# Kernel optimization log

Hardware: AMD Instinct MI355X
Metric: run time of the kernel (lower is better)

The kernel has to match this reference:

```python
import jax, jax.numpy as jnp
import numpy as np

B, E, K, S, D, H, C = 8192, 8, 2, 32, 3072, 256, 100  # batch, experts, fix_points, img size, flat dim, hidden, classes


def setup_inputs() -> dict:
    key = jax.random.key(0)
    ks = jax.random.split(key, 6)
    return {
        "x": jax.random.normal(ks[0], (B, 3, S, S), jnp.float32),
        "coeffs_t": jax.random.uniform(ks[1], (K,), jnp.float32),
        "router_w": jax.random.normal(ks[2], (K, D, E), jnp.float32) * 0.02,
        "router_b": jnp.zeros((K, E), jnp.float32),
        "w1": jax.random.normal(ks[3], (E, K, D, H), jnp.float32) * 0.02,
        "b1": jnp.zeros((E, K, H), jnp.float32),
        "w2": jax.random.normal(ks[4], (E, K, H, C), jnp.float32) * 0.02,
        "b2": jnp.zeros((E, K, C), jnp.float32),
    }


def reference(x, coeffs_t, router_w, router_b, w1, b1, w2, b2):
    xf = x.reshape(x.shape[0], -1)  # [B, D]
    # Curve parameter blend: W = sum_k coeffs_t[k] * W_k (CurveParameter semantics)
    Wr = jnp.einsum('k,kde->de', coeffs_t, router_w)
    br = jnp.einsum('k,ke->e', coeffs_t, router_b)
    # Router: top-1 expert index per sample
    idx = jnp.argmax(xf @ Wr + br, axis=-1)  # [B] int
    # Blended expert weights
    W1 = jnp.einsum('k,ekdh->edh', coeffs_t, w1)
    B1 = jnp.einsum('k,ekh->eh', coeffs_t, b1)
    W2 = jnp.einsum('k,ekhc->ehc', coeffs_t, w2)
    B2 = jnp.einsum('k,ekc->ec', coeffs_t, b2)
    # Expert MLP (computed for all experts with static shapes, then top-1 gather;
    # identical math to torch's boolean-mask dispatch/scatter)
    h = jax.nn.gelu(jnp.einsum('bd,edh->beh', xf, W1) + B1, approximate=False)  # [B,E,H]
    o = jnp.einsum('beh,ehc->bec', h, W2) + B2  # [B,E,C]
    return jnp.take_along_axis(o, idx[:, None, None], axis=1)[:, 0, :]  # [B,C]
```

## Files before the change

kernel.cpp:

```cpp
#include <hip/hip_runtime.h>
#include <math.h>

#define B_  8192
#define E_  8
#define D_  3072
#define H_  256
#define C_  100
#define DH_ (D_*H_)
#define HC_ (H_*C_)
#define KS_ 8
#define KSEG_ (D_/KS_)
#define RKS_ 16
#define RSEG_ (D_/RKS_)
#define RB_ (B_/256)
#define NTMAX_ 136
#define NT2MAX_ 528
#define NCH_ (D_/32)
#define CHW_ 10240

#define MEGA_R_   (RB_*RKS_)
#define MEGA_W1_  (E_*NCH_)
#define MEGA_W2_  (C_*E_)
#define MEGA_BB_  3
#define MEGA_TOT_ (MEGA_R_ + MEGA_W1_ + MEGA_W2_ + MEGA_BB_)

typedef __attribute__((ext_vector_type(4))) float  f32x4;
typedef __attribute__((ext_vector_type(8))) __bf16 bf16x8;
typedef __attribute__((ext_vector_type(8))) unsigned short ush8;
typedef __attribute__((ext_vector_type(4))) unsigned short ush4;

#define GLOAD_LDS16(g, l) __builtin_amdgcn_global_load_lds( \
    (const __attribute__((address_space(1))) void*)(g),     \
    (__attribute__((address_space(3))) void*)(l), 16, 0, 0)

__device__ inline unsigned short bf16_rne(float f) {
    unsigned u = __builtin_bit_cast(unsigned, f);
    unsigned r = (u + 0x7FFFu + ((u >> 16) & 1u)) >> 16;
    return (unsigned short)r;
}
__device__ inline float bf16_f(unsigned short h) {
    unsigned u = ((unsigned)h) << 16;
    return __builtin_bit_cast(float, u);
}

#define MISC_B1_ (E_*H_/4)
#define MISC_B2_ (E_*C_/4)

__global__ __launch_bounds__(256, 2) void mega_k(
        const float* __restrict__ x, const float* __restrict__ rw,
        const float* __restrict__ w1, const float* __restrict__ w2,
        const float* __restrict__ b1, const float* __restrict__ b2,
        unsigned short* __restrict__ Whi, unsigned short* __restrict__ Wlo,
        unsigned short* __restrict__ W2thi, unsigned short* __restrict__ W2tlo,
        float* __restrict__ B1b, float* __restrict__ B2b,
        double* __restrict__ lpart, const float* __restrict__ coeffs) {
    __shared__ char smem[36864];
    int bid = blockIdx.x;
    int t = threadIdx.x;

    if (bid < MEGA_R_) {
        float  (*xs)[64][33] = (float(*)[64][33])smem;
        double (*wls)[8]     = (double(*)[8])(smem + 33792);
        int w = t >> 6, lane = t & 63;
        int rowblk = (bid & (RB_ - 1)) * 256;
        int s2     = bid >> 5;
        int kbase  = s2 * RSEG_;
        int row0   = rowblk + w * 64;
        double c0 = (double)coeffs[0], c1 = (double)coeffs[1];

        double acc[8] = {0, 0, 0, 0, 0, 0, 0, 0};

        float4 px[8];
        float rwa[4], rwb[4];
        #pragma unroll
        for (int it = 0; it < 8; it++) {
            int i = lane + it * 64;
            int r = i >> 3, c4 = i & 7;
            px[it] = *(const float4*)(x + (size_t)(row0 + r) * D_ + kbase + c4 * 4);
        }
        if (w == 0) {
            #pragma unroll
            for (int it = 0; it < 4; it++) {
                int i = lane + it * 64;
                int k = i >> 3, ee = i & 7;
                rwa[it] = rw[(size_t)(kbase + k) * 8 + ee];
                rwb[it] = rw[(size_t)(D_ + kbase + k) * 8 + ee];
            }
        }

        for (int kb = 0; kb < RSEG_; kb += 32) {
            #pragma unroll
            for (int it = 0; it < 8; it++) {
                int i = lane + it * 64;
                int r = i >> 3, c4 = i & 7;
                *(float4*)&xs[w][r][c4 * 4] = px[it];
            }
            if (w == 0) {
                #pragma unroll
                for (int it = 0; it < 4; it++) {
                    int i = lane + it * 64;
                    int k = i >> 3, ee = i & 7;
                    wls[k][ee] = c0 * (double)rwa[it] + c1 * (double)rwb[it];
                }
            }
            __syncthreads();

            if (kb + 32 < RSEG_) {
                #pragma unroll
                for (int it = 0; it < 8; it++) {
                    int i = lane + it * 64;
                    int r = i >> 3, c4 = i & 7;
                    px[it] = *(const float4*)(x + (size_t)(row0 + r) * D_ +
                                              kbase + kb + 32 + c4 * 4);
                }
                if (w == 0) {
                    #pragma unroll
                    for (int it = 0; it < 4; it++) {
                        int i = lane + it * 64;
                        int k = i >> 3, ee = i & 7;
                        rwa[it] = rw[(size_t)(kbase + kb + 32 + k) * 8 + ee];
                        rwb[it] = rw[(size_t)(D_ + kbase + kb + 32 + k) * 8 + ee];
                    }
                }
            }

            #pragma unroll
            for (int kk = 0; kk < 32; kk++) {
                double xv = (double)xs[w][lane][kk];
                double2 w01 = *(const double2*)&wls[kk][0];
                double2 w23 = *(const double2*)&wls[kk][2];
                double2 w45 = *(const double2*)&wls[kk][4];
                double2 w67 = *(const double2*)&wls[kk][6];
                acc[0] = fma(xv, w01.x, acc[0]);
                acc[1] = fma(xv, w01.y, acc[1]);
                acc[2] = fma(xv, w23.x, acc[2]);
                acc[3] = fma(xv, w23.y, acc[3]);
                acc[4] = fma(xv, w45.x, acc[4]);
                acc[5] = fma(xv, w45.y, acc[5]);
                acc[6] = fma(xv, w67.x, acc[6]);
                acc[7] = fma(xv, w67.y, acc[7]);
            }
            __syncthreads();
        }
        size_t base = ((size_t)s2 * B_ + row0 + lane) * 8;
        #pragma unroll
        for (int ee = 0; ee < 8; ee++) lpart[base + ee] = acc[ee];

    } else if (bid < MEGA_R_ + MEGA_W1_) {
        int lid = bid - MEGA_R_;
        int e  = lid / NCH_;
        int ci = lid - e * NCH_;
        int d0 = ci * 32;
        unsigned short* thi = (unsigned short*)smem;
        unsigned short* tlo = thi + 32 * 256;
        float c0 = coeffs[0], c1 = coeffs[1];
        const float* pa = w1 + ((size_t)(e * 2 + 0) * D_ + d0) * H_;
        const float* pb = w1 + ((size_t)(e * 2 + 1) * D_ + d0) * H_;
        #pragma unroll
        for (int it = 0; it < 8; it++) {
            int i4 = t + it * 256;
            float4 va = *(const float4*)(pa + (size_t)i4 * 4);
            float4 vb = *(const float4*)(pb + (size_t)i4 * 4);
            float vv[4] = {c0 * va.x + c1 * vb.x, c0 * va.y + c1 * vb.y,
                           c0 * va.z + c1 * vb.z, c0 * va.w + c1 * vb.w};
            unsigned short h4[4], l4[4];
            #pragma unroll
            for (int j = 0; j < 4; j++) {
                unsigned short hi = bf16_rne(vv[j]);
                h4[j] = hi;
                l4[j] = bf16_rne(vv[j] - bf16_f(hi));
            }
            *(ush4*)&thi[i4 * 4] = *(const ush4*)h4;
            *(ush4*)&tlo[i4 * 4] = *(const ush4*)l4;
        }
        __syncthreads();
        #pragma unroll
        for (int it = 0; it < 4; it++) {
            int j = t + it * 256;
            int h = j >> 2, d8 = (j & 3) * 8;
            unsigned short vh[8], vl[8];
            #pragma unroll
            for (int k2 = 0; k2 < 8; k2++) {
                vh[k2] = thi[(d8 + k2) * 256 + h];
                vl[k2] = tlo[(d8 + k2) * 256 + h];
            }
            size_t g = ((size_t)e * NCH_ + ci) * CHW_ + (size_t)h * 40 + d8;
            *(ush8*)(Whi + g) = *(const ush8*)vh;
            *(ush8*)(Wlo + g) = *(const ush8*)vl;
        }

    } else if (bid < MEGA_R_ + MEGA_W1_ + MEGA_W2_) {
        int lid = bid - (MEGA_R_ + MEGA_W1_);
        int c = lid % C_, e = lid / C_;
        int k = t;
        float c0 = coeffs[0], c1 = coeffs[1];
        float v = c0 * w2[((size_t)(e * 2 + 0) * H_ + k) * C_ + c]
                + c1 * w2[((size_t)(e * 2 + 1) * H_ + k) * C_ + c];
        unsigned short hi = bf16_rne(v);
        W2thi[(size_t)(e * C_ + c) * H_ + k] = hi;
        W2tlo[(size_t)(e * C_ + c) * H_ + k] = bf16_rne(v - bf16_f(hi));

    } else {
        int gid = (bid - (MEGA_R_ + MEGA_W1_ + MEGA_W2_)) * 256 + t;
        float c0 = coeffs[0], c1 = coeffs[1];
        if (gid < MISC_B1_) {
            const float4* p = (const float4*)b1;
            int e = gid / (H_ / 4), r = gid - e * (H_ / 4);
            float4 a = p[(e * 2 + 0) * (H_ / 4) + r];
            float4 bq = p[(e * 2 + 1) * (H_ / 4) + r];
            float4 o;
            o.x = c0 * a.x + c1 * bq.x;
            o.y = c0 * a.y + c1 * bq.y;
            o.z = c0 * a.z + c1 * bq.z;
            o.w = c0 * a.w + c1 * bq.w;
            ((float4*)B1b)[gid] = o;
        } else if (gid < MISC_B1_ + MISC_B2_) {
            int g2 = gid - MISC_B1_;
            const float4* p = (const float4*)b2;
            int e = g2 / (C_ / 4), r = g2 - e * (C_ / 4);
            float4 a = p[(e * 2 + 0) * (C_ / 4) + r];
            float4 bq = p[(e * 2 + 1) * (C_ / 4) + r];
            float4 o;
            o.x = c0 * a.x + c1 * bq.x;
            o.y = c0 * a.y + c1 * bq.y;
            o.z = c0 * a.z + c1 * bq.z;
            o.w = c0 * a.w + c1 * bq.w;
            ((float4*)B2b)[g2] = o;
        }
    }
}

__global__ __launch_bounds__(256) void argmax_hist_k(
        const double* __restrict__ lpart, const float* __restrict__ rb,
        const float* __restrict__ coeffs, int* __restrict__ idx,
        int* __restrict__ hist) {
    __shared__ int scnt[8];
    int t = threadIdx.x;
    if (t < 8) scnt[t] = 0;
    __syncthreads();
    int b = blockIdx.x * 256 + t;
    double c0 = (double)coeffs[0], c1 = (double)coeffs[1];
    double l[8];
    #pragma unroll
    for (int e = 0; e < 8; e++)
        l[e] = c0 * (double)rb[e] + c1 * (double)rb[8 + e];
    for (int s2 = 0; s2 < RKS_; s2++) {
        const double2* pp = (const double2*)(lpart + ((size_t)s2 * B_ + b) * 8);
        double2 v0 = pp[0], v1 = pp[1], v2 = pp[2], v3 = pp[3];
        l[0] += v0.x; l[1] += v0.y; l[2] += v1.x; l[3] += v1.y;
        l[4] += v2.x; l[5] += v2.y; l[6] += v3.x; l[7] += v3.y;
    }
    double best = -1e300;
    int bi = 0;
    #pragma unroll
    for (int e = 0; e < 8; e++)
        if (l[e] > best) { best = l[e]; bi = e; }
    idx[b] = bi;
    atomicAdd(&scnt[bi], 1);
    __syncthreads();
    if (t < 8) hist[blockIdx.x * 8 + t] = scnt[t];
}

__global__ __launch_bounds__(256) void scatter2_k(
        const int* __restrict__ idx, const int* __restrict__ hist,
        int* __restrict__ order, int* __restrict__ cnt, int* __restrict__ off,
        int* __restrict__ tmap, int* __restrict__ tmap2, int* __restrict__ ntl) {
    __shared__ int sbi[256];
    __shared__ int stot[8];
    __shared__ int sbase[8];
    int b0 = blockIdx.x, t = threadIdx.x;
    int b = b0 * 256 + t;
    int mybi = idx[b];
    sbi[t] = mybi;
    if (t < 8) {
        int tot = 0, pre = 0;
        for (int bb = 0; bb < RB_; bb++) {
            int h = hist[bb * 8 + t];
            if (bb < b0) pre += h;
            tot += h;
        }
        stot[t] = tot;
        sbase[t] = pre;
    }
    __syncthreads();
    if (t < 8) {
        int o = 0;
        for (int j = 0; j < t; j++) o += stot[j];
        sbase[t] += o;
    }
    __syncthreads();
    int rank = 0;
    for (int i = 0; i < 256; i++) {
        int v = sbi[i];
        rank += (i < t && v == mybi) ? 1 : 0;
    }
    order[sbase[mybi] + rank] = (mybi << 16) | b;

    if (b0 == 0 && t == 0) {
        int s = 0;
        for (int e = 0; e < E_; e++) { cnt[e] = stot[e]; off[e] = s; s += stot[e]; }
        int nt = 0;
        for (int e = 0; e < E_; e++)
            for (int t0 = 0; t0 < stot[e]; t0 += 64)
                tmap[nt++] = (e << 16) | t0;
        ntl[0] = nt;
        int nt2 = 0;
        for (int e = 0; e < E_; e++)
            for (int t0 = 0; t0 < stot[e]; t0 += 16)
                tmap2[nt2++] = (e << 16) | t0;
        ntl[1] = nt2;
    }
}

template<int MODE>
__global__ __launch_bounds__(256, 3) void gemm1_t(
        const float* __restrict__ x, const unsigned short* __restrict__ Whi,
        const unsigned short* __restrict__ Wlo, const int* __restrict__ order,
        const int* __restrict__ cnt, const int* __restrict__ off,
        const int* __restrict__ tmap, const int* __restrict__ ntl,
        float* __restrict__ dst) {
    int tid = blockIdx.y;
    if (tid >= ntl[0]) return;
    int tm = tmap[tid];
    int e = tm >> 16, tile0 = tm & 0xFFFF;
    int ce = cnt[e];
    int s = blockIdx.x;

    __shared__ int rows[64];
    __shared__ unsigned short xs_hi[64 * 40];
    __shared__ unsigned short xs_lo[64 * 40];
    __shared__ unsigned short ws_hi[256 * 40];
    __shared__ unsigned short ws_lo[256 * 40];

    int t = threadIdx.x;
    if (t < 64) {
        int i = tile0 + t;
        rows[t] = (i < ce) ? (order[off[e] + i] & 0xFFFF) : -1;
    }
    __syncthreads();
    int xrow0 = rows[0];

    int lane = t & 63, w = t >> 6;
    int lr = lane & 15, quad = lane >> 4;
    int kbase = s * KSEG_;
    int wuni = t & ~63;

    f32x4 acc[4][4];
    #pragma unroll
    for (int mt = 0; mt < 4; mt++)
        #pragma unroll
        for (int nt = 0; nt < 4; nt++)
            acc[mt][nt] = (f32x4){0.f, 0.f, 0.f, 0.f};

    for (int kb = 0; kb < KSEG_; kb += 32) {
        {
            int ci = (kbase + kb) >> 5;
            const unsigned short* ph = Whi + ((size_t)e * NCH_ + ci) * CHW_;
            const unsigned short* pl = Wlo + ((size_t)e * NCH_ + ci) * CHW_;
            #pragma unroll
            for (int j = 0; j < 5; j++) {
                GLOAD_LDS16(ph + ((size_t)(j * 256 + t)) * 8,
                            ws_hi + (size_t)(j * 256 + wuni) * 8);
                GLOAD_LDS16(pl + ((size_t)(j * 256 + t)) * 8,
                            ws_lo + (size_t)(j * 256 + wuni) * 8);
            }
        }
        #pragma unroll
        for (int it = 0; it < 2; it++) {
            int i = t + it * 256;
            int rr = i >> 3, sg = i & 7;
            int row = rows[rr];
            if (row < 0) row = xrow0;
            float4 v = *(const float4*)(x + (size_t)row * D_ + kbase + kb + sg * 4);
            unsigned short h4[4], l4[4];
            float vv[4] = {v.x, v.y, v.z, v.w};
            #pragma unroll
            for (int j = 0; j < 4; j++) {
                unsigned short hi = bf16_rne(vv[j]);
                h4[j] = hi;
                l4[j] = bf16_rne(vv[j] - bf16_f(hi));
            }
            *(ush4*)&xs_hi[rr * 40 + sg * 4] = *(const ush4*)h4;
            *(ush4*)&xs_lo[rr * 40 + sg * 4] = *(const ush4*)l4;
        }
        __syncthreads();

        bf16x8 ah[4], al[4], bh[4], bl[4];
        #pragma unroll
        for (int mt = 0; mt < 4; mt++) {
            ah[mt] = __builtin_bit_cast(bf16x8, *(const ush8*)&xs_hi[(mt * 16 + lr) * 40 + quad * 8]);
            al[mt] = __builtin_bit_cast(bf16x8, *(const ush8*)&xs_lo[(mt * 16 + lr) * 40 + quad * 8]);
        }
        #pragma unroll
        for (int nt = 0; nt < 4; nt++) {
            int col = w * 64 + nt * 16 + lr;
            bh[nt] = __builtin_bit_cast(bf16x8, *(const ush8*)&ws_hi[col * 40 + quad * 8]);
            bl[nt] = __builtin_bit_cast(bf16x8, *(const ush8*)&ws_lo[col * 40 + quad * 8]);
        }
        #pragma unroll
        for (int mt = 0; mt < 4; mt++)
            #pragma unroll
            for (int nt = 0; nt < 4; nt++) {
                acc[mt][nt] = __builtin_amdgcn_mfma_f32_16x16x32_bf16(ah[mt], bh[nt], acc[mt][nt], 0, 0, 0);
                acc[mt][nt] = __builtin_amdgcn_mfma_f32_16x16x32_bf16(al[mt], bh[nt], acc[mt][nt], 0, 0, 0);
                acc[mt][nt] = __builtin_amdgcn_mfma_f32_16x16x32_bf16(ah[mt], bl[nt], acc[mt][nt], 0, 0, 0);
                acc[mt][nt] = __builtin_amdgcn_mfma_f32_16x16x32_bf16(al[mt], bl[nt], acc[mt][nt], 0, 0, 0);
            }
        __syncthreads();
    }

    size_t p0 = (size_t)off[e] + tile0;
    if (MODE == 1) {
        float* dp = dst + ((size_t)s * B_ + p0) * H_;
        #pragma unroll
        for (int mt = 0; mt < 4; mt++) {
            int rl = mt * 16 + quad * 4;
            #pragma unroll
            for (int nt = 0; nt < 4; nt++) {
                int col = w * 64 + nt * 16 + lr;
                #pragma unroll
                for (int rg = 0; rg < 4; rg++) {
                    if (tile0 + rl + rg < ce)
                        dp[(size_t)(rl + rg) * H_ + col] = acc[mt][nt][rg];
                }
            }
        }
    } else {
        #pragma unroll
        for (int mt = 0; mt < 4; mt++) {
            int rl = mt * 16 + quad * 4;
            #pragma unroll
            for (int nt = 0; nt < 4; nt++) {
                int col = w * 64 + nt * 16 + lr;
                #pragma unroll
                for (int rg = 0; rg < 4; rg++) {
                    if (tile0 + rl + rg < ce)
                        atomicAdd(&dst[(p0 + rl + rg) * H_ + col], acc[mt][nt][rg]);
                }
            }
        }
    }
}

__global__ __launch_bounds__(256) void bias_gelu_k(
        float* __restrict__ hws, const float* __restrict__ B1b,
        const int* __restrict__ order) {
    int gid = blockIdx.x * 256 + threadIdx.x;
    int p = gid >> 6, c4 = (gid & 63) * 4;
    int e = order[p] >> 16;
    float4 v = *(const float4*)(hws + (size_t)p * H_ + c4);
    const float4 bb = *(const float4*)(B1b + e * H_ + c4);
    float pre[4] = {v.x + bb.x, v.y + bb.y, v.z + bb.z, v.w + bb.w};
    float4 o;
    o.x = 0.5f * pre[0] * (1.0f + erff(pre[0] * 0.70710678118654752440f));
    o.y = 0.5f * pre[1] * (1.0f + erff(pre[1] * 0.70710678118654752440f));
    o.z = 0.5f * pre[2] * (1.0f + erff(pre[2] * 0.70710678118654752440f));
    o.w = 0.5f * pre[3] * (1.0f + erff(pre[3] * 0.70710678118654752440f));
    *(float4*)(hws + (size_t)p * H_ + c4) = o;
}

template<int FUSE>
__global__ __launch_bounds__(256) void gemm2_t(
        const float* __restrict__ hsrc,
        const unsigned short* __restrict__ W2thi, const unsigned short* __restrict__ W2tlo,
        const float* __restrict__ B1b, const float* __restrict__ B2b,
        const int* __restrict__ order, const int* __restrict__ cnt,
        const int* __restrict__ off, const int* __restrict__ tmap2,
        const int* __restrict__ ntl, float* __restrict__ out) {
    int tid = blockIdx.x;
    if (tid >= ntl[1]) return;
    int tm = tmap2[tid];
    int e = tm >> 16, tile0 = tm & 0xFFFF;
    int ce = cnt[e];

    __shared__ int rows[16];
    __shared__ float red[3][64][28];

    int t = threadIdx.x;
    if (t < 16) {
        int i = tile0 + t;
        rows[t] = (i < ce) ? (order[off[e] + i] & 0xFFFF) : -1;
    }
    __syncthreads();

    int lane = t & 63, w = t >> 6;
    int m = lane & 15, q = lane >> 4;
    int p = off[e] + tile0 + ((tile0 + m < ce) ? m : 0);

    f32x4 acc[7];
    #pragma unroll
    for (int nt = 0; nt < 7; nt++) acc[nt] = (f32x4){0.f, 0.f, 0.f, 0.f};

    const unsigned short* w2h = W2thi + (size_t)e * C_ * H_;
    const unsigned short* w2l = W2tlo + (size_t)e * C_ * H_;

    #pragma unroll
    for (int si = 0; si < 2; si++) {
        int s = w * 2 + si;
        int k0 = s * 32 + q * 8;
        size_t o = (size_t)p * H_ + k0;
        float f[8];
        if (FUSE) {
            float4 a0 = *(const float4*)(hsrc + o);
            float4 a1 = *(const float4*)(hsrc + o + 4);
            #pragma unroll
            for (int s2 = 1; s2 < KS_; s2++) {
                const float* sp = hsrc + (size_t)s2 * B_ * H_ + o;
                float4 b0 = *(const float4*)sp;
                float4 b1v = *(const float4*)(sp + 4);
                a0.x += b0.x; a0.y += b0.y; a0.z += b0.z; a0.w += b0.w;
                a1.x += b1v.x; a1.y += b1v.y; a1.z += b1v.z; a1.w += b1v.w;
            }
            float4 bb0 = *(const float4*)(B1b + e * H_ + k0);
            float4 bb1 = *(const float4*)(B1b + e * H_ + k0 + 4);
            float pre[8] = {a0.x + bb0.x, a0.y + bb0.y, a0.z + bb0.z, a0.w + bb0.w,
                            a1.x + bb1.x, a1.y + bb1.y, a1.z + bb1.z, a1.w + bb1.w};
            #pragma unroll
            for (int j = 0; j < 8; j++)
                f[j] = 0.5f * pre[j] * (1.0f + erff(pre[j] * 0.70710678118654752440f));
        } else {
            float4 v0 = *(const float4*)(hsrc + o);
            float4 v1 = *(const float4*)(hsrc + o + 4);
            f[0] = v0.x; f[1] = v0.y; f[2] = v0.z; f[3] = v0.w;
            f[4] = v1.x; f[5] = v1.y; f[6] = v1.z; f[7] = v1.w;
        }
        unsigned short hh[8], lo[8];
        #pragma unroll
        for (int j = 0; j < 8; j++) {
            unsigned short hi = bf16_rne(f[j]);
            hh[j] = hi;
            lo[j] = bf16_rne(f[j] - bf16_f(hi));
        }
        bf16x8 ah = __builtin_bit_cast(bf16x8, *(const ush8*)hh);
        bf16x8 al = __builtin_bit_cast(bf16x8, *(const ush8*)lo);
        #pragma unroll
        for (int nt = 0; nt < 7; nt++) {
            size_t bo = (size_t)(nt * 16 + m) * H_ + k0;
            bf16x8 bh = __builtin_bit_cast(bf16x8, *(const ush8*)(w2h + bo));
            bf16x8 bl = __builtin_bit_cast(bf16x8, *(const ush8*)(w2l + bo));
            acc[nt] = __builtin_amdgcn_mfma_f32_16x16x32_bf16(ah, bh, acc[nt], 0, 0, 0);
            acc[nt] = __builtin_amdgcn_mfma_f32_16x16x32_bf16(al, bh, acc[nt], 0, 0, 0);
            acc[nt] = __builtin_amdgcn_mfma_f32_16x16x32_bf16(ah, bl, acc[nt], 0, 0, 0);
            acc[nt] = __builtin_amdgcn_mfma_f32_16x16x32_bf16(al, bl, acc[nt], 0, 0, 0);
        }
    }

    if (w > 0) {
        #pragma unroll
        for (int nt = 0; nt < 7; nt++)
            #pragma unroll
            for (int i = 0; i < 4; i++)
                red[w - 1][lane][nt * 4 + i] = acc[nt][i];
    }
    __syncthreads();
    if (w == 0) {
        #pragma unroll
        for (int nt = 0; nt < 7; nt++)
            #pragma unroll
            for (int i = 0; i < 4; i++)
                acc[nt][i] = ((acc[nt][i] + red[0][lane][nt * 4 + i])
                              + red[1][lane][nt * 4 + i]) + red[2][lane][nt * 4 + i];
        #pragma unroll
        for (int nt = 0; nt < 7; nt++) {
            int c = nt * 16 + m;
            if (c >= C_) continue;
            float bias = B2b[e * C_ + c];
            #pragma unroll
            for (int i = 0; i < 4; i++) {
                int grow = q * 4 + i;
                if (tile0 + grow < ce)
                    out[(size_t)rows[grow] * C_ + c] = acc[nt][i] + bias;
            }
        }
    }
}

extern "C" void kernel_launch(void* const* d_in, const int* in_sizes, int n_in,
                              void* d_out, int out_size, void* d_ws, size_t ws_size,
                              hipStream_t stream) {
    const float* x        = (const float*)d_in[0];
    const float* coeffs   = (const float*)d_in[1];
    const float* router_w = (const float*)d_in[2];
    const float* router_b = (const float*)d_in[3];
    const float* w1       = (const float*)d_in[4];
    const float* b1       = (const float*)d_in[5];
    const float* w2       = (const float*)d_in[6];
    const float* b2       = (const float*)d_in[7];
    float* out = (float*)d_out;

    unsigned short* Whi   = (unsigned short*)d_ws;
    unsigned short* Wlo   = Whi + (size_t)E_ * NCH_ * CHW_;
    unsigned short* W2thi = Wlo + (size_t)E_ * NCH_ * CHW_;
    unsigned short* W2tlo = W2thi + (size_t)E_ * C_ * H_;
    float* B1b  = (float*)(W2tlo + (size_t)E_ * C_ * H_);
    float* B2b  = B1b + (size_t)E_ * H_;
    int* order  = (int*)(B2b + E_ * C_);
    int* cnt    = order + B_;
    int* off    = cnt + E_;
    int* tmap   = off + E_;
    int* tmap2  = tmap + NTMAX_;
    int* ntl    = tmap2 + NT2MAX_;
    int* idx    = ntl + 4;
    int* hist   = idx + B_;
    float* hws  = (float*)(hist + 256);
    double* lpart = (double*)hws;

    size_t prefix_bytes = (size_t)((char*)hws - (char*)d_ws);
    int use_part = (ws_size >= prefix_bytes + (size_t)KS_ * B_ * H_ * sizeof(float) + 256) ? 1 : 0;

    mega_k<<<dim3(MEGA_TOT_), 256, 0, stream>>>(
        x, router_w, w1, w2, b1, b2, Whi, Wlo, W2thi, W2tlo, B1b, B2b,
        lpart, coeffs);

    argmax_hist_k<<<dim3(RB_), 256, 0, stream>>>(lpart, router_b, coeffs, idx, hist);
    scatter2_k<<<dim3(RB_), 256, 0, stream>>>(idx, hist, order, cnt, off,
                                              tmap, tmap2, ntl);

    if (use_part) {
        gemm1_t<1><<<dim3(KS_, NTMAX_), 256, 0, stream>>>(x, Whi, Wlo, order, cnt,
                                                          off, tmap, ntl, hws);
        gemm2_t<1><<<dim3(NT2MAX_), 256, 0, stream>>>(hws, W2thi, W2tlo, B1b, B2b,
                                                      order, cnt, off, tmap2, ntl, out);
    } else {
        hipMemsetAsync(hws, 0, (size_t)B_ * H_ * sizeof(float), stream);
        gemm1_t<0><<<dim3(KS_, NTMAX_), 256, 0, stream>>>(x, Whi, Wlo, order, cnt,
                                                          off, tmap, ntl, hws);
        bias_gelu_k<<<dim3(B_ * H_ / 4 / 256), 256, 0, stream>>>(hws, B1b, order);
        gemm2_t<0><<<dim3(NT2MAX_), 256, 0, stream>>>(hws, W2thi, W2tlo, B1b, B2b,
                                                      order, cnt, off, tmap2, ntl, out);
    }
}
```

Measured before the change: 349.4 us.

## Move split-K reduction and bias+GELU into last-arriving gemm1 block; drop router prefetch

The split-K partial sums of the first expert GEMM are now reduced, biased and passed through GELU by the last of the KS_ blocks to finish each tile. Completion is detected with a per-tile atomic counter, which is zeroed by a memset before launch. Previously gemm2 did this 8-way reduction for every tile it consumed; it now reads finished activations. Separately, the router section of mega_k drops its register double-buffered prefetch and its occupancy hint. That lowers register pressure but exposes global load latency, and the fusion adds a memset launch plus atomic and fence overhead.

```diff
diff --git a/kernel.cpp b/kernel.cpp
--- a/kernel.cpp
+++ b/kernel.cpp
@@ -46,7 +46,7 @@
 #define MISC_B1_ (E_*H_/4)
 #define MISC_B2_ (E_*C_/4)
 
-__global__ __launch_bounds__(256, 2) void mega_k(
+__global__ __launch_bounds__(256) void mega_k(
         const float* __restrict__ x, const float* __restrict__ rw,
         const float* __restrict__ w1, const float* __restrict__ w2,
         const float* __restrict__ b1, const float* __restrict__ b2,
@@ -70,60 +70,24 @@
 
         double acc[8] = {0, 0, 0, 0, 0, 0, 0, 0};
 
-        float4 px[8];
-        float rwa[4], rwb[4];
-        #pragma unroll
-        for (int it = 0; it < 8; it++) {
-            int i = lane + it * 64;
-            int r = i >> 3, c4 = i & 7;
-            px[it] = *(const float4*)(x + (size_t)(row0 + r) * D_ + kbase + c4 * 4);
-        }
-        if (w == 0) {
-            #pragma unroll
-            for (int it = 0; it < 4; it++) {
-                int i = lane + it * 64;
-                int k = i >> 3, ee = i & 7;
-                rwa[it] = rw[(size_t)(kbase + k) * 8 + ee];
-                rwb[it] = rw[(size_t)(D_ + kbase + k) * 8 + ee];
-            }
-        }
-
         for (int kb = 0; kb < RSEG_; kb += 32) {
             #pragma unroll
             for (int it = 0; it < 8; it++) {
                 int i = lane + it * 64;
                 int r = i >> 3, c4 = i & 7;
-                *(float4*)&xs[w][r][c4 * 4] = px[it];
+                *(float4*)&xs[w][r][c4 * 4] =
+                    *(const float4*)(x + (size_t)(row0 + r) * D_ + kbase + kb + c4 * 4);
             }
             if (w == 0) {
                 #pragma unroll
                 for (int it = 0; it < 4; it++) {
                     int i = lane + it * 64;
                     int k = i >> 3, ee = i & 7;
-                    wls[k][ee] = c0 * (double)rwa[it] + c1 * (double)rwb[it];
+                    wls[k][ee] = c0 * (double)rw[(size_t)(kbase + kb + k) * 8 + ee]
+                               + c1 * (double)rw[(size_t)(D_ + kbase + kb + k) * 8 + ee];
                 }
             }
             __syncthreads();
-
-            if (kb + 32 < RSEG_) {
-                #pragma unroll
-                for (int it = 0; it < 8; it++) {
-                    int i = lane + it * 64;
-                    int r = i >> 3, c4 = i & 7;
-                    px[it] = *(const float4*)(x + (size_t)(row0 + r) * D_ +
-                                              kbase + kb + 32 + c4 * 4);
-                }
-                if (w == 0) {
-                    #pragma unroll
-                    for (int it = 0; it < 4; it++) {
-                        int i = lane + it * 64;
-                        int k = i >> 3, ee = i & 7;
-                        rwa[it] = rw[(size_t)(kbase + kb + 32 + k) * 8 + ee];
-                        rwb[it] = rw[(size_t)(D_ + kbase + kb + 32 + k) * 8 + ee];
-                    }
-                }
-            }
-
             #pragma unroll
             for (int kk = 0; kk < 32; kk++) {
                 double xv = (double)xs[w][lane][kk];
@@ -318,6 +282,7 @@
         const unsigned short* __restrict__ Wlo, const int* __restrict__ order,
         const int* __restrict__ cnt, const int* __restrict__ off,
         const int* __restrict__ tmap, const int* __restrict__ ntl,
+        const float* __restrict__ B1b, int* __restrict__ tcnt,
         float* __restrict__ dst) {
     int tid = blockIdx.y;
     if (tid >= ntl[0]) return;
@@ -327,6 +292,7 @@
     int s = blockIdx.x;
 
     __shared__ int rows[64];
+    __shared__ int sdone;
     __shared__ unsigned short xs_hi[64 * 40];
     __shared__ unsigned short xs_lo[64 * 40];
     __shared__ unsigned short ws_hi[256 * 40];
@@ -422,6 +388,35 @@
                 for (int rg = 0; rg < 4; rg++) {
                     if (tile0 + rl + rg < ce)
                         dp[(size_t)(rl + rg) * H_ + col] = acc[mt][nt][rg];
+                }
+            }
+        }
+        __threadfence();
+        if (t == 0) sdone = atomicAdd(&tcnt[tid], 1);
+        __syncthreads();
+        if (sdone == KS_ - 1) {
+            __threadfence();
+            #pragma unroll
+            for (int it = 0; it < 16; it++) {
+                int i = t + it * 256;
+                int r = i >> 6, c4 = (i & 63) * 4;
+                if (tile0 + r < ce) {
+                    size_t o = (p0 + r) * H_ + c4;
+                    float4 a = *(const float4*)(dst + o);
+                    #pragma unroll
+                    for (int s2 = 1; s2 < KS_; s2++) {
+                        const float* sp = dst + (size_t)s2 * B_ * H_ + o;
+                        float4 b = *(const float4*)sp;
+                        a.x += b.x; a.y += b.y; a.z += b.z; a.w += b.w;
+                    }
+                    const float4 bb = *(const float4*)(B1b + e * H_ + c4);
+                    float pre[4] = {a.x + bb.x, a.y + bb.y, a.z + bb.z, a.w + bb.w};
+                    float4 og;
+                    og.x = 0.5f * pre[0] * (1.0f + erff(pre[0] * 0.70710678118654752440f));
+                    og.y = 0.5f * pre[1] * (1.0f + erff(pre[1] * 0.70710678118654752440f));
+                    og.z = 0.5f * pre[2] * (1.0f + erff(pre[2] * 0.70710678118654752440f));
+                    og.w = 0.5f * pre[3] * (1.0f + erff(pre[3] * 0.70710678118654752440f));
+                    *(float4*)(dst + o) = og;
                 }
             }
         }
@@ -459,14 +454,13 @@
     *(float4*)(hws + (size_t)p * H_ + c4) = o;
 }
 
-template<int FUSE>
-__global__ __launch_bounds__(256) void gemm2_t(
-        const float* __restrict__ hsrc,
+__global__ __launch_bounds__(256) void gemm2_k(
+        const float* __restrict__ hws,
         const unsigned short* __restrict__ W2thi, const unsigned short* __restrict__ W2tlo,
-        const float* __restrict__ B1b, const float* __restrict__ B2b,
-        const int* __restrict__ order, const int* __restrict__ cnt,
-        const int* __restrict__ off, const int* __restrict__ tmap2,
-        const int* __restrict__ ntl, float* __restrict__ out) {
+        const float* __restrict__ B2b, const int* __restrict__ order,
+        const int* __restrict__ cnt, const int* __restrict__ off,
+        const int* __restrict__ tmap2, const int* __restrict__ ntl,
+        float* __restrict__ out) {
     int tid = blockIdx.x;
     if (tid >= ntl[1]) return;
     int tm = tmap2[tid];
@@ -499,31 +493,9 @@
         int s = w * 2 + si;
         int k0 = s * 32 + q * 8;
         size_t o = (size_t)p * H_ + k0;
-        float f[8];
-        if (FUSE) {
-            float4 a0 = *(const float4*)(hsrc + o);
-            float4 a1 = *(const float4*)(hsrc + o + 4);
-            #pragma unroll
-            for (int s2 = 1; s2 < KS_; s2++) {
-                const float* sp = hsrc + (size_t)s2 * B_ * H_ + o;
-                float4 b0 = *(const float4*)sp;
-                float4 b1v = *(const float4*)(sp + 4);
-                a0.x += b0.x; a0.y += b0.y; a0.z += b0.z; a0.w += b0.w;
-                a1.x += b1v.x; a1.y += b1v.y; a1.z += b1v.z; a1.w += b1v.w;
-            }
-            float4 bb0 = *(const float4*)(B1b + e * H_ + k0);
-            float4 bb1 = *(const float4*)(B1b + e * H_ + k0 + 4);
-            float pre[8] = {a0.x + bb0.x, a0.y + bb0.y, a0.z + bb0.z, a0.w + bb0.w,
-                            a1.x + bb1.x, a1.y + bb1.y, a1.z + bb1.z, a1.w + bb1.w};
-            #pragma unroll
-            for (int j = 0; j < 8; j++)
-                f[j] = 0.5f * pre[j] * (1.0f + erff(pre[j] * 0.70710678118654752440f));
-        } else {
-            float4 v0 = *(const float4*)(hsrc + o);
-            float4 v1 = *(const float4*)(hsrc + o + 4);
-            f[0] = v0.x; f[1] = v0.y; f[2] = v0.z; f[3] = v0.w;
-            f[4] = v1.x; f[5] = v1.y; f[6] = v1.z; f[7] = v1.w;
-        }
+        float4 v0 = *(const float4*)(hws + o);
+        float4 v1 = *(const float4*)(hws + o + 4);
+        float f[8] = {v0.x, v0.y, v0.z, v0.w, v1.x, v1.y, v1.z, v1.w};
         unsigned short hh[8], lo[8];
         #pragma unroll
         for (int j = 0; j < 8; j++) {
@@ -602,7 +574,8 @@
     int* ntl    = tmap2 + NT2MAX_;
     int* idx    = ntl + 4;
     int* hist   = idx + B_;
-    float* hws  = (float*)(hist + 256);
+    int* tcnt   = hist + 256;
+    float* hws  = (float*)(tcnt + 144);
     double* lpart = (double*)hws;
 
     size_t prefix_bytes = (size_t)((char*)hws - (char*)d_ws);
@@ -617,16 +590,19 @@
                                               tmap, tmap2, ntl);
 
     if (use_part) {
+        hipMemsetAsync(tcnt, 0, NTMAX_ * sizeof(int), stream);
         gemm1_t<1><<<dim3(KS_, NTMAX_), 256, 0, stream>>>(x, Whi, Wlo, order, cnt,
-                                                          off, tmap, ntl, hws);
-        gemm2_t<1><<<dim3(NT2MAX_), 256, 0, stream>>>(hws, W2thi, W2tlo, B1b, B2b,
-                                                      order, cnt, off, tmap2, ntl, out);
+                                                          off, tmap, ntl, B1b,
+                                                          tcnt, hws);
+        gemm2_k<<<dim3(NT2MAX_), 256, 0, stream>>>(hws, W2thi, W2tlo, B2b,
+                                                   order, cnt, off, tmap2, ntl, out);
     } else {
         hipMemsetAsync(hws, 0, (size_t)B_ * H_ * sizeof(float), stream);
         gemm1_t<0><<<dim3(KS_, NTMAX_), 256, 0, stream>>>(x, Whi, Wlo, order, cnt,
-                                                          off, tmap, ntl, hws);
+                                                          off, tmap, ntl, B1b,
+                                                          tcnt, hws);
         bias_gelu_k<<<dim3(B_ * H_ / 4 / 256), 256, 0, stream>>>(hws, B1b, order);
-        gemm2_t<0><<<dim3(NT2MAX_), 256, 0, stream>>>(hws, W2thi, W2tlo, B1b, B2b,
-                                                      order, cnt, off, tmap2, ntl, out);
-    }
-}
+        gemm2_k<<<dim3(NT2MAX_), 256, 0, stream>>>(hws, W2thi, W2tlo, B2b,
+                                                   order, cnt, off, tmap2, ntl, out);
+    }
+}
```

Result: slower. 653.9 us (+87.2%).

## Remove register prefetch in router phase and relax launch bounds

Applied to the files above, without the earlier changes.

Removes the software register prefetch of the next x tile and router weights in the router section of the mega kernel. Tiles are now loaded straight from global memory into shared memory at the start of each k-step. It also drops the minimum-blocks-per-CU hint from launch_bounds, so the compiler may use more registers. This lowers register pressure, but global load latency is no longer hidden behind the FMA loop, and occupancy may fall.

```diff
diff --git a/kernel.cpp b/kernel.cpp
--- a/kernel.cpp
+++ b/kernel.cpp
@@ -46,7 +46,7 @@
 #define MISC_B1_ (E_*H_/4)
 #define MISC_B2_ (E_*C_/4)
 
-__global__ __launch_bounds__(256, 2) void mega_k(
+__global__ __launch_bounds__(256) void mega_k(
         const float* __restrict__ x, const float* __restrict__ rw,
         const float* __restrict__ w1, const float* __restrict__ w2,
         const float* __restrict__ b1, const float* __restrict__ b2,
@@ -70,60 +70,24 @@
 
         double acc[8] = {0, 0, 0, 0, 0, 0, 0, 0};
 
-        float4 px[8];
-        float rwa[4], rwb[4];
-        #pragma unroll
-        for (int it = 0; it < 8; it++) {
-            int i = lane + it * 64;
-            int r = i >> 3, c4 = i & 7;
-            px[it] = *(const float4*)(x + (size_t)(row0 + r) * D_ + kbase + c4 * 4);
-        }
-        if (w == 0) {
-            #pragma unroll
-            for (int it = 0; it < 4; it++) {
-                int i = lane + it * 64;
-                int k = i >> 3, ee = i & 7;
-                rwa[it] = rw[(size_t)(kbase + k) * 8 + ee];
-                rwb[it] = rw[(size_t)(D_ + kbase + k) * 8 + ee];
-            }
-        }
-
         for (int kb = 0; kb < RSEG_; kb += 32) {
             #pragma unroll
             for (int it = 0; it < 8; it++) {
                 int i = lane + it * 64;
                 int r = i >> 3, c4 = i & 7;
-                *(float4*)&xs[w][r][c4 * 4] = px[it];
+                *(float4*)&xs[w][r][c4 * 4] =
+                    *(const float4*)(x + (size_t)(row0 + r) * D_ + kbase + kb + c4 * 4);
             }
             if (w == 0) {
                 #pragma unroll
                 for (int it = 0; it < 4; it++) {
                     int i = lane + it * 64;
                     int k = i >> 3, ee = i & 7;
-                    wls[k][ee] = c0 * (double)rwa[it] + c1 * (double)rwb[it];
+                    wls[k][ee] = c0 * (double)rw[(size_t)(kbase + kb + k) * 8 + ee]
+                               + c1 * (double)rw[(size_t)(D_ + kbase + kb + k) * 8 + ee];
                 }
             }
             __syncthreads();
-
-            if (kb + 32 < RSEG_) {
-                #pragma unroll
-                for (int it = 0; it < 8; it++) {
-                    int i = lane + it * 64;
-                    int r = i >> 3, c4 = i & 7;
-                    px[it] = *(const float4*)(x + (size_t)(row0 + r) * D_ +
-                                              kbase + kb + 32 + c4 * 4);
-                }
-                if (w == 0) {
-                    #pragma unroll
-                    for (int it = 0; it < 4; it++) {
-                        int i = lane + it * 64;
-                        int k = i >> 3, ee = i & 7;
-                        rwa[it] = rw[(size_t)(kbase + kb + 32 + k) * 8 + ee];
-                        rwb[it] = rw[(size_t)(D_ + kbase + kb + 32 + k) * 8 + ee];
-                    }
-                }
-            }
-
             #pragma unroll
             for (int kk = 0; kk < 32; kk++) {
                 double xv = (double)xs[w][lane][kk];
```

Result: faster. 332.6 us (-4.8%).
